# Optimization experiments

Measured on AMD Instinct MI355X. Metric: run time of the kernel, lower is better.

Reference implementation:

```python
import jax, jax.numpy as jnp
import numpy as np

B, N, D, H = 1, 4096, 1024, 16
HD = D // H  # head_dim = 64


def setup_inputs() -> dict:
    key = jax.random.key(0)
    ks = jax.random.split(key, 5)
    s = 0.02
    return {
        "x": jax.random.normal(ks[0], (B, N, D), dtype=jnp.float32),
        "Wq": jax.random.normal(ks[1], (D, D), dtype=jnp.float32) * s,
        "Wk": jax.random.normal(ks[2], (D, D), dtype=jnp.float32) * s,
        "Wv": jax.random.normal(ks[3], (D, D), dtype=jnp.float32) * s,
        "Wo": jax.random.normal(ks[4], (D, D), dtype=jnp.float32) * s,
        "bo": jnp.zeros((D,), dtype=jnp.float32),
    }


def reference(x, Wq, Wk, Wv, Wo, bo):
    b, n, d = x.shape
    # QKV projections -> [b, h, n, hd]
    def proj(W):
        return jnp.einsum("bnd,de->bne", x, W).reshape(b, n, H, HD).transpose(0, 2, 1, 3)
    q, k, v = proj(Wq), proj(Wk), proj(Wv)
    # Scores [b, h, n, n] with causal mask (matches masked_fill with triu(diag=1))
    scores = jnp.einsum("bhqd,bhkd->bhqk", q, k)
    causal = jnp.tril(jnp.ones((n, n), dtype=bool))
    scores = jnp.where(causal, scores, -jnp.inf)
    attn = jax.nn.softmax(scores / jnp.sqrt(jnp.float32(HD)), axis=-1)
    # dropout p=0.0 -> identity
    ctx = jnp.einsum("bhqk,bhkd->bhqd", attn, v)
    ctx = ctx.transpose(0, 2, 1, 3).reshape(b, n, d)
    return jnp.einsum("bnd,de->bne", ctx, Wo) + bo
```

## Files before the change

kernel.cpp:

```cpp
#include <hip/hip_runtime.h>


#define N_TOK 4096
#define DMODEL 1024
#define NH 16
#define HDIM 64

typedef __bf16 bf16x8 __attribute__((ext_vector_type(8)));
typedef short short4v __attribute__((ext_vector_type(4)));
typedef unsigned int uint2v __attribute__((ext_vector_type(2)));
typedef float f32x4 __attribute__((ext_vector_type(4)));

__device__ __forceinline__ unsigned short f2bf(float f) {
  unsigned u = __builtin_bit_cast(unsigned, f);
  u += 0x7FFFu + ((u >> 16) & 1u);
  return (unsigned short)(u >> 16);
}

__device__ __forceinline__ float bf2f(unsigned short u) {
  unsigned x = (unsigned)u << 16;
  return __builtin_bit_cast(float, x);
}

__device__ __forceinline__ unsigned pack2bf(float f0, float f1) {
  unsigned a = __builtin_bit_cast(unsigned, f0);
  unsigned b = __builtin_bit_cast(unsigned, f1);
  a += 0x7FFFu + ((a >> 16) & 1u);
  b += 0x7FFFu + ((b >> 16) & 1u);
  return (a >> 16) | (b & 0xFFFF0000u);
}

__device__ __forceinline__ f32x4 mfma16x16x16(short4v a, short4v b, f32x4 c) {
#if defined(__HIP_DEVICE_COMPILE__)
#if __has_builtin(__builtin_amdgcn_mfma_f32_16x16x16bf16_1k)
  return __builtin_amdgcn_mfma_f32_16x16x16bf16_1k(a, b, c, 0, 0, 0);
#else
  asm volatile("v_mfma_f32_16x16x16_bf16 %0, %1, %2, %0\n\ts_nop 7\n\ts_nop 1"
               : "+v"(c) : "v"(a), "v"(b));
  return c;
#endif
#else
  return c;
#endif
}

__device__ __forceinline__ void gll16(const unsigned short* g, unsigned short* l) {
#if defined(__HIP_DEVICE_COMPILE__)
  __builtin_amdgcn_global_load_lds((const __attribute__((address_space(1))) void*)g,
                                   (__attribute__((address_space(3))) void*)l, 16, 0, 0);
#endif
}

__global__ __launch_bounds__(256) void cast_x_kernel(const float* __restrict__ x,
                                                     unsigned short* __restrict__ xb) {
  const int i = (blockIdx.x * 256 + threadIdx.x) * 4;
  float4 v = *(const float4*)(x + i);
  ushort4 o;
  o.x = f2bf(v.x); o.y = f2bf(v.y); o.z = f2bf(v.z); o.w = f2bf(v.w);
  *(ushort4*)(xb + i) = o;
}

__global__ __launch_bounds__(256) void transpose_w_kernel(
    const float* __restrict__ Wq, const float* __restrict__ Wk,
    const float* __restrict__ Wv, const float* __restrict__ Wo,
    unsigned short* __restrict__ Wqt, unsigned short* __restrict__ Wkt,
    unsigned short* __restrict__ Wvt, unsigned short* __restrict__ Wot) {
  __shared__ float t[32][33];
  const float* src;
  unsigned short* dst;
  switch (blockIdx.z) {
    case 0: src = Wq; dst = Wqt; break;
    case 1: src = Wk; dst = Wkt; break;
    case 2: src = Wv; dst = Wvt; break;
    default: src = Wo; dst = Wot; break;
  }
  const int tx = threadIdx.x, ty = threadIdx.y;
  const int x = blockIdx.x * 32 + tx;
  const int y0 = blockIdx.y * 32;
#pragma unroll
  for (int i = 0; i < 32; i += 8) t[ty + i][tx] = src[(y0 + ty + i) * DMODEL + x];
  __syncthreads();
  const int ox = blockIdx.y * 32 + tx;
  const int oy0 = blockIdx.x * 32;
#pragma unroll
  for (int i = 0; i < 32; i += 8) dst[(oy0 + ty + i) * DMODEL + ox] = f2bf(t[tx][ty + i]);
}

__global__ __launch_bounds__(256) void gemm_qkv_kernel(
    const unsigned short* __restrict__ xb,
    const unsigned short* __restrict__ Wqt, const unsigned short* __restrict__ Wkt,
    const unsigned short* __restrict__ Wvt,
    unsigned short* __restrict__ Qg, unsigned short* __restrict__ Kg,
    unsigned short* __restrict__ Vg) {
  __shared__ unsigned short As[128 * 32];
  __shared__ unsigned short Bs[128 * 32];
  const int z = blockIdx.z;
  const unsigned short* Bmat = (z == 0) ? Wqt : ((z == 1) ? Wkt : Wvt);
  const int tid = threadIdx.x, lane = tid & 63, wv = tid >> 6;
  const int quad = lane >> 4, l15 = lane & 15;
  const int wm = wv >> 1, wn = wv & 1;
  const int tm0 = blockIdx.y * 128, tn0 = blockIdx.x * 128;
  const int lrow = lane >> 2, lcol = (lane & 3) * 8;
  const f32x4 zero4 = {0.f, 0.f, 0.f, 0.f};
  f32x4 acc[4][4];
#pragma unroll
  for (int i = 0; i < 4; ++i)
#pragma unroll
    for (int j = 0; j < 4; ++j) acc[i][j] = zero4;

  for (int kb = 0; kb < DMODEL; kb += 32) {
#pragma unroll
    for (int r = 0; r < 2; ++r) {
      const int row0 = r * 64 + wv * 16;
      gll16(&xb[(tm0 + row0 + lrow) * DMODEL + kb + lcol], &As[row0 * 32]);
      gll16(&Bmat[(tn0 + row0 + lrow) * DMODEL + kb + lcol], &Bs[row0 * 32]);
    }
    __syncthreads();
    bf16x8 af[4], bfr[4];
#pragma unroll
    for (int i = 0; i < 4; ++i) {
      af[i]  = *(const bf16x8*)&As[(wm * 64 + i * 16 + l15) * 32 + quad * 8];
      bfr[i] = *(const bf16x8*)&Bs[(wn * 64 + i * 16 + l15) * 32 + quad * 8];
    }
#pragma unroll
    for (int mt = 0; mt < 4; ++mt)
#pragma unroll
      for (int nt = 0; nt < 4; ++nt)
        acc[mt][nt] = __builtin_amdgcn_mfma_f32_16x16x32_bf16(af[mt], bfr[nt], acc[mt][nt], 0, 0, 0);
    __syncthreads();
  }

  const float qs = 0.125f * 1.44269504088896f;
#pragma unroll
  for (int mt = 0; mt < 4; ++mt)
#pragma unroll
    for (int nt = 0; nt < 4; ++nt)
#pragma unroll
      for (int r = 0; r < 4; ++r) {
        const int row = tm0 + wm * 64 + mt * 16 + quad * 4 + r;
        const int col = tn0 + wn * 64 + nt * 16 + l15;
        const float v = acc[mt][nt][r];
        const int hh = col >> 6, hd = col & 63;
        if (z == 0)      Qg[(hh * N_TOK + row) * HDIM + hd] = f2bf(v * qs);
        else if (z == 1) Kg[(hh * N_TOK + row) * HDIM + hd] = f2bf(v);
        else             Vg[(hh * N_TOK + row) * HDIM + hd] = f2bf(v);
      }
}

__global__ __launch_bounds__(256) void v_transpose_kernel(
    const unsigned short* __restrict__ Vg, unsigned short* __restrict__ Vtg) {
  __shared__ unsigned short t[64][72];
  const int h = blockIdx.y;
  const int n0 = blockIdx.x * 64;
  const int tx = threadIdx.x & 63, ty = threadIdx.x >> 6;
  const unsigned short* src = Vg + (h * N_TOK + n0) * HDIM;
#pragma unroll
  for (int i = 0; i < 64; i += 4) t[i + ty][tx] = src[(i + ty) * HDIM + tx];
  __syncthreads();
  unsigned short* dst = Vtg + h * HDIM * N_TOK + n0;
#pragma unroll
  for (int i = 0; i < 64; i += 4) dst[(i + ty) * N_TOK + tx] = t[tx][i + ty];
}

#define TRW 68

__device__ static const unsigned char T_TAB[63] = {
    10, 11, 12, 13, 14, 15, 16, 17, 18, 19, 20, 21, 22, 23, 24, 25, 26, 27, 28, 29, 30,
    31, 21, 22, 23, 24, 25, 26, 27, 28, 29, 30, 31,
    9, 20, 31, 8, 19, 30, 7, 18, 29, 6, 17, 28, 5, 16, 27,
    4, 15, 26, 3, 14, 25, 2, 13, 24, 1, 12, 23, 0, 11, 22};
__device__ static const unsigned char G_TAB[63] = {
    0, 0, 0, 0, 0, 0, 0, 0, 0, 0, 0, 0, 0, 0, 0, 0, 0, 0, 0, 0, 0,
    0, 1, 1, 1, 1, 1, 1, 1, 1, 1, 1, 1,
    0, 1, 2, 0, 1, 2, 0, 1, 2, 0, 1, 2, 0, 1, 2,
    0, 1, 2, 0, 1, 2, 0, 1, 2, 0, 1, 2, 0, 1, 2};

__device__ __forceinline__ void stage_kv(
    const unsigned short* __restrict__ Kh, const unsigned short* __restrict__ Vh,
    int kv0, char* buf, int wv, int lane) {
  unsigned short* Ksb = (unsigned short*)buf;
  unsigned short* Vsb = (unsigned short*)(buf + 8192);
  const int r8 = lane >> 3, g = lane & 7;
  const int sw = ((g ^ r8) * 8);
#pragma unroll
  for (int i = 0; i < 2; ++i) {
    const int row = wv * 16 + i * 8;
    gll16(&Kh[(kv0 + row + r8) * HDIM + sw], &Ksb[row * 64]);
    gll16(&Vh[(row + r8) * N_TOK + kv0 + sw], &Vsb[row * 64]);
  }
}

template <bool MASKED>
__device__ __forceinline__ void attn_step(
    int kvs, int qw, int quad, int l15,
    const unsigned short* __restrict__ Ks, const unsigned short* __restrict__ Vs,
    const bf16x8 (&qf)[2][2], f32x4 (&o)[2][4], float (&l_)[2]) {
  const f32x4 zero4 = {0.f, 0.f, 0.f, 0.f};
  const int s = l15 & 7;
  f32x4 c[2][4];
#pragma unroll
  for (int mt = 0; mt < 4; ++mt) {
    const unsigned short* kp = &Ks[(mt * 16 + l15) * 64];
    const int g0 = (quad ^ s) * 8;
    const bf16x8 kf0 = *(const bf16x8*)(kp + g0);
    const bf16x8 kf1 = *(const bf16x8*)(kp + (g0 ^ 32));
#pragma unroll
    for (int qt = 0; qt < 2; ++qt) {
      c[qt][mt] = __builtin_amdgcn_mfma_f32_16x16x32_bf16(kf0, qf[qt][0], zero4, 0, 0, 0);
      c[qt][mt] = __builtin_amdgcn_mfma_f32_16x16x32_bf16(kf1, qf[qt][1], c[qt][mt], 0, 0, 0);
    }
  }
  short4v pb[2][4];
#pragma unroll
  for (int qt = 0; qt < 2; ++qt) {
    const int q = qw + qt * 16 + l15;
    float ls = 0.f;
#pragma unroll
    for (int mt = 0; mt < 4; ++mt) {
      float p[4];
#pragma unroll
      for (int r = 0; r < 4; ++r) {
        float v = c[qt][mt][r];
        if (MASKED) v = ((kvs + mt * 16 + quad * 4 + r) <= q) ? v : -3e38f;
        p[r] = exp2f(v);
      }
      ls += (p[0] + p[1]) + (p[2] + p[3]);
      uint2v w;
      w.x = pack2bf(p[0], p[1]);
      w.y = pack2bf(p[2], p[3]);
      pb[qt][mt] = __builtin_bit_cast(short4v, w);
    }
    l_[qt] += ls;
  }
#pragma unroll
  for (int mt = 0; mt < 4; ++mt)
#pragma unroll
    for (int dt = 0; dt < 4; ++dt) {
      const int gv = (((2 * mt + (quad >> 1)) ^ s) * 8) + (quad & 1) * 4;
      const short4v vfx = *(const short4v*)&Vs[(dt * 16 + l15) * 64 + gv];
      o[0][dt] = mfma16x16x16(vfx, pb[0][mt], o[0][dt]);
      o[1][dt] = mfma16x16x16(vfx, pb[1][mt], o[1][dt]);
    }
}

__global__ __launch_bounds__(256, 3) void attn_kernel(
    const unsigned short* __restrict__ Qg, const unsigned short* __restrict__ Kg,
    const unsigned short* __restrict__ Vtg, unsigned short* __restrict__ ctx,
    unsigned short* __restrict__ part_o, float* __restrict__ part_l) {
  __shared__ __align__(16) char smem[34816];
  const int tid = threadIdx.x, lane = tid & 63, wv = tid >> 6;
  const int quad = lane >> 4, l15 = lane & 15;

  const int u = blockIdx.x >> 4;
  const int h = blockIdx.x & 15;
  const int t = T_TAB[u], g = G_TAB[u];
  const int c0 = g * 11;
  const int cend = (c0 + 10 < t) ? (c0 + 10) : t;
  const int mlen = 2 * (cend - c0 + 1);
  const bool multi = (t >= 11);
  const int qb = t * 128, qw = qb + wv * 32;

  const unsigned short* Qh = Qg + h * N_TOK * HDIM;
  const unsigned short* Kh = Kg + h * N_TOK * HDIM;
  const unsigned short* Vh = Vtg + h * HDIM * N_TOK;

  bf16x8 qf[2][2];
#pragma unroll
  for (int qt = 0; qt < 2; ++qt)
#pragma unroll
    for (int hh = 0; hh < 2; ++hh)
      qf[qt][hh] = *(const bf16x8*)&Qh[(qw + qt * 16 + l15) * HDIM + hh * 32 + quad * 8];

  const f32x4 zero4 = {0.f, 0.f, 0.f, 0.f};
  f32x4 o[2][4];
#pragma unroll
  for (int qt = 0; qt < 2; ++qt)
#pragma unroll
    for (int dt = 0; dt < 4; ++dt) o[qt][dt] = zero4;
  float l_[2] = {0.f, 0.f};

  const int kvbase = c0 << 7;
  stage_kv(Kh, Vh, kvbase, smem, wv, lane);
  int cur = 0;
#pragma unroll 1
  for (int mc = 0; mc < mlen; ++mc) {
    const int kv0 = kvbase + mc * 64;
    __syncthreads();
    if (mc + 1 < mlen)
      stage_kv(Kh, Vh, kv0 + 64, smem + (cur ^ 1) * 16384, wv, lane);
    const unsigned short* Ksb = (const unsigned short*)(smem + cur * 16384);
    const unsigned short* Vsb = (const unsigned short*)(smem + cur * 16384 + 8192);
    if (kv0 <= qw + 31) {
      if (kv0 + 63 <= qw)
        attn_step<false>(kv0, qw, quad, l15, Ksb, Vsb, qf, o, l_);
      else
        attn_step<true>(kv0, qw, quad, l15, Ksb, Vsb, qf, o, l_);
    }
    cur ^= 1;
  }
  __syncthreads();

  float* Tr = (float*)(smem + wv * (32 * TRW * 4));
  const int tq = lane >> 1, half = lane & 1;
  if (!multi) {
#pragma unroll
    for (int qt = 0; qt < 2; ++qt) {
      float l = l_[qt];
      l += __shfl_xor(l, 16, 64);
      l += __shfl_xor(l, 32, 64);
      const float inv = 1.0f / l;
#pragma unroll
      for (int dt = 0; dt < 4; ++dt) {
        f32x4 v = o[qt][dt] * inv;
        *(f32x4*)&Tr[(qt * 16 + l15) * TRW + dt * 16 + quad * 4] = v;
      }
    }
    unsigned short* dst = &ctx[(qb + wv * 32 + tq) * DMODEL + h * HDIM + half * 32];
    const float* src = &Tr[tq * TRW + half * 32];
#pragma unroll
    for (int j = 0; j < 4; ++j) {
      const float* s8 = src + j * 8;
      uint4 w;
      w.x = pack2bf(s8[0], s8[1]);
      w.y = pack2bf(s8[2], s8[3]);
      w.z = pack2bf(s8[4], s8[5]);
      w.w = pack2bf(s8[6], s8[7]);
      *(uint4*)(dst + j * 8) = w;
    }
  } else {
    const int slot = (h * 21 + (t - 11)) * 3 + g;
#pragma unroll
    for (int qt = 0; qt < 2; ++qt) {
      float l = l_[qt];
      l += __shfl_xor(l, 16, 64);
      l += __shfl_xor(l, 32, 64);
      if (quad == 0) part_l[slot * 128 + wv * 32 + qt * 16 + l15] = l;
#pragma unroll
      for (int dt = 0; dt < 4; ++dt)
        *(f32x4*)&Tr[(qt * 16 + l15) * TRW + dt * 16 + quad * 4] = o[qt][dt];
    }
    unsigned short* dst = part_o + (size_t)slot * 8192 + (wv * 32 + tq) * 64 + half * 32;
    const float* src = &Tr[tq * TRW + half * 32];
#pragma unroll
    for (int j = 0; j < 4; ++j) {
      const float* s8 = src + j * 8;
      uint4 w;
      w.x = pack2bf(s8[0], s8[1]);
      w.y = pack2bf(s8[2], s8[3]);
      w.z = pack2bf(s8[4], s8[5]);
      w.w = pack2bf(s8[6], s8[7]);
      *(uint4*)(dst + j * 8) = w;
    }
  }
}

__global__ __launch_bounds__(256) void merge_kernel(
    const unsigned short* __restrict__ part_o, const float* __restrict__ part_l,
    unsigned short* __restrict__ ctx) {
  const int b = blockIdx.x;
  const int h = b / 21, tt = b % 21;
  const int t = tt + 11;
  const int ng = t / 11 + 1;
  const int tid = threadIdx.x;
  const int q = tid >> 1, half = tid & 1;
  const int s0 = (h * 21 + tt) * 3;
  float l = 0.f;
  for (int g = 0; g < ng; ++g) l += part_l[(s0 + g) * 128 + q];
  const float inv = 1.0f / l;
  unsigned short* dst = &ctx[(t * 128 + q) * DMODEL + h * HDIM + half * 32];
#pragma unroll
  for (int j = 0; j < 4; ++j) {
    float acc[8] = {0.f, 0.f, 0.f, 0.f, 0.f, 0.f, 0.f, 0.f};
    for (int g = 0; g < ng; ++g) {
      const uint4 w = *(const uint4*)(part_o + (size_t)(s0 + g) * 8192 + q * 64 + half * 32 + j * 8);
      const unsigned short* us = (const unsigned short*)&w;
#pragma unroll
      for (int e = 0; e < 8; ++e) acc[e] += bf2f(us[e]);
    }
    uint4 w;
    w.x = pack2bf(acc[0] * inv, acc[1] * inv);
    w.y = pack2bf(acc[2] * inv, acc[3] * inv);
    w.z = pack2bf(acc[4] * inv, acc[5] * inv);
    w.w = pack2bf(acc[6] * inv, acc[7] * inv);
    *(uint4*)(dst + j * 8) = w;
  }
}

__global__ __launch_bounds__(256) void gemm_out_kernel(
    const unsigned short* __restrict__ ctxb, const unsigned short* __restrict__ Wot,
    const float* __restrict__ bo, float* __restrict__ out) {
  __shared__ unsigned short As[128 * 32];
  __shared__ unsigned short Bs[128 * 32];
  const int tid = threadIdx.x, lane = tid & 63, wv = tid >> 6;
  const int quad = lane >> 4, l15 = lane & 15;
  const int wm = wv >> 1, wn = wv & 1;
  const int tm0 = blockIdx.y * 128, tn0 = blockIdx.x * 128;
  const int lrow = lane >> 2, lcol = (lane & 3) * 8;
  const f32x4 zero4 = {0.f, 0.f, 0.f, 0.f};
  f32x4 acc[4][4];
#pragma unroll
  for (int i = 0; i < 4; ++i)
#pragma unroll
    for (int j = 0; j < 4; ++j) acc[i][j] = zero4;

  for (int kb = 0; kb < DMODEL; kb += 32) {
#pragma unroll
    for (int r = 0; r < 2; ++r) {
      const int row0 = r * 64 + wv * 16;
      gll16(&ctxb[(tm0 + row0 + lrow) * DMODEL + kb + lcol], &As[row0 * 32]);
      gll16(&Wot[(tn0 + row0 + lrow) * DMODEL + kb + lcol], &Bs[row0 * 32]);
    }
    __syncthreads();
    bf16x8 af[4], bfr[4];
#pragma unroll
    for (int i = 0; i < 4; ++i) {
      af[i]  = *(const bf16x8*)&As[(wm * 64 + i * 16 + l15) * 32 + quad * 8];
      bfr[i] = *(const bf16x8*)&Bs[(wn * 64 + i * 16 + l15) * 32 + quad * 8];
    }
#pragma unroll
    for (int mt = 0; mt < 4; ++mt)
#pragma unroll
      for (int nt = 0; nt < 4; ++nt)
        acc[mt][nt] = __builtin_amdgcn_mfma_f32_16x16x32_bf16(af[mt], bfr[nt], acc[mt][nt], 0, 0, 0);
    __syncthreads();
  }
#pragma unroll
  for (int mt = 0; mt < 4; ++mt)
#pragma unroll
    for (int nt = 0; nt < 4; ++nt)
#pragma unroll
      for (int r = 0; r < 4; ++r) {
        const int row = tm0 + wm * 64 + mt * 16 + quad * 4 + r;
        const int col = tn0 + wn * 64 + nt * 16 + l15;
        out[row * DMODEL + col] = acc[mt][nt][r] + bo[col];
      }
}

extern "C" void kernel_launch(void* const* d_in, const int* in_sizes, int n_in,
                              void* d_out, int out_size, void* d_ws, size_t ws_size,
                              hipStream_t stream) {
  const float* x  = (const float*)d_in[0];
  const float* Wq = (const float*)d_in[1];
  const float* Wk = (const float*)d_in[2];
  const float* Wv = (const float*)d_in[3];
  const float* Wo = (const float*)d_in[4];
  const float* bo = (const float*)d_in[5];
  float* out = (float*)d_out;

  char* ws = (char*)d_ws;
  unsigned short* xb  = (unsigned short*)(ws);
  unsigned short* Wqt = (unsigned short*)(ws + 8388608);
  unsigned short* Wkt = (unsigned short*)(ws + 8388608 + 2097152);
  unsigned short* Wvt = (unsigned short*)(ws + 8388608 + 2 * 2097152);
  unsigned short* Wot = (unsigned short*)(ws + 8388608 + 3 * 2097152);
  unsigned short* Qg  = (unsigned short*)(ws + 16777216);
  unsigned short* Kg  = (unsigned short*)(ws + 25165824);
  unsigned short* Vtg = (unsigned short*)(ws + 33554432);
  unsigned short* ctx = xb;
  unsigned short* part_o = (unsigned short*)(ws + 41943040);
  float* part_l = (float*)(ws + 58458112);
  unsigned short* Vg = part_o;

  cast_x_kernel<<<N_TOK * DMODEL / (256 * 4), 256, 0, stream>>>(x, xb);
  transpose_w_kernel<<<dim3(32, 32, 4), dim3(32, 8), 0, stream>>>(Wq, Wk, Wv, Wo, Wqt, Wkt, Wvt, Wot);
  gemm_qkv_kernel<<<dim3(DMODEL / 128, N_TOK / 128, 3), 256, 0, stream>>>(xb, Wqt, Wkt, Wvt, Qg, Kg, Vg);
  v_transpose_kernel<<<dim3(N_TOK / 64, NH), 256, 0, stream>>>(Vg, Vtg);
  attn_kernel<<<1008, 256, 0, stream>>>(Qg, Kg, Vtg, ctx, part_o, part_l);
  merge_kernel<<<336, 256, 0, stream>>>(part_o, part_l, ctx);
  gemm_out_kernel<<<dim3(DMODEL / 128, N_TOK / 128), 256, 0, stream>>>(ctx, Wot, bo, out);
}
```

Before: 242.0 us.

## Fuse prep kernels, write V transposed from QKV GEMM, use packed bf16 convert

Merges the x cast and weight transpose into one launch and drops the separate V transpose kernel: the QKV GEMM now transposes V tiles through shared memory and writes Vt directly with vector stores. The attention softmax also uses the hardware packed bf16 conversion when the builtin exists. This removes two kernel launches and a full round trip of V through global memory. The cost is extra shared memory (about 17KB) in the GEMM, which may lower its occupancy, plus added barriers in the V epilogue.

Result: faster. 235.4 us (-2.7%).

```diff
diff --git a/kernel.cpp b/kernel.cpp
--- a/kernel.cpp
+++ b/kernel.cpp
@@ -7,6 +7,7 @@
 #define HDIM 64
 
 typedef __bf16 bf16x8 __attribute__((ext_vector_type(8)));
+typedef __bf16 bf16x2v __attribute__((ext_vector_type(2)));
 typedef short short4v __attribute__((ext_vector_type(4)));
 typedef unsigned int uint2v __attribute__((ext_vector_type(2)));
 typedef float f32x4 __attribute__((ext_vector_type(4)));
@@ -28,6 +29,15 @@
   a += 0x7FFFu + ((a >> 16) & 1u);
   b += 0x7FFFu + ((b >> 16) & 1u);
   return (a >> 16) | (b & 0xFFFF0000u);
+}
+
+__device__ __forceinline__ unsigned packpk(float f0, float f1) {
+#if defined(__HIP_DEVICE_COMPILE__) && __has_builtin(__builtin_amdgcn_cvt_pk_bf16_f32)
+  bf16x2v r = __builtin_amdgcn_cvt_pk_bf16_f32(f0, f1);
+  return __builtin_bit_cast(unsigned, r);
+#else
+  return pack2bf(f0, f1);
+#endif
 }
 
 __device__ __forceinline__ f32x4 mfma16x16x16(short4v a, short4v b, f32x4 c) {
@@ -51,37 +61,41 @@
 #endif
 }
 
-__global__ __launch_bounds__(256) void cast_x_kernel(const float* __restrict__ x,
-                                                     unsigned short* __restrict__ xb) {
-  const int i = (blockIdx.x * 256 + threadIdx.x) * 4;
-  float4 v = *(const float4*)(x + i);
-  ushort4 o;
-  o.x = f2bf(v.x); o.y = f2bf(v.y); o.z = f2bf(v.z); o.w = f2bf(v.w);
-  *(ushort4*)(xb + i) = o;
-}
-
-__global__ __launch_bounds__(256) void transpose_w_kernel(
+__global__ __launch_bounds__(256) void prep_kernel(
+    const float* __restrict__ x, unsigned short* __restrict__ xb,
     const float* __restrict__ Wq, const float* __restrict__ Wk,
     const float* __restrict__ Wv, const float* __restrict__ Wo,
     unsigned short* __restrict__ Wqt, unsigned short* __restrict__ Wkt,
     unsigned short* __restrict__ Wvt, unsigned short* __restrict__ Wot) {
+  const int bx = blockIdx.x;
+  if (bx < 4096) {
+    const int i = (bx * 256 + threadIdx.x) * 4;
+    float4 v = *(const float4*)(x + i);
+    ushort4 o;
+    o.x = f2bf(v.x); o.y = f2bf(v.y); o.z = f2bf(v.z); o.w = f2bf(v.w);
+    *(ushort4*)(xb + i) = o;
+    return;
+  }
   __shared__ float t[32][33];
+  const int r = bx - 4096;
+  const int z = r >> 10, rem = r & 1023;
+  const int by = rem >> 5, bxx = rem & 31;
   const float* src;
   unsigned short* dst;
-  switch (blockIdx.z) {
+  switch (z) {
     case 0: src = Wq; dst = Wqt; break;
     case 1: src = Wk; dst = Wkt; break;
     case 2: src = Wv; dst = Wvt; break;
     default: src = Wo; dst = Wot; break;
   }
-  const int tx = threadIdx.x, ty = threadIdx.y;
-  const int x = blockIdx.x * 32 + tx;
-  const int y0 = blockIdx.y * 32;
-#pragma unroll
-  for (int i = 0; i < 32; i += 8) t[ty + i][tx] = src[(y0 + ty + i) * DMODEL + x];
+  const int tx = threadIdx.x & 31, ty = threadIdx.x >> 5;
+  const int xx = bxx * 32 + tx;
+  const int y0 = by * 32;
+#pragma unroll
+  for (int i = 0; i < 32; i += 8) t[ty + i][tx] = src[(y0 + ty + i) * DMODEL + xx];
   __syncthreads();
-  const int ox = blockIdx.y * 32 + tx;
-  const int oy0 = blockIdx.x * 32;
+  const int ox = by * 32 + tx;
+  const int oy0 = bxx * 32;
 #pragma unroll
   for (int i = 0; i < 32; i += 8) dst[(oy0 + ty + i) * DMODEL + ox] = f2bf(t[tx][ty + i]);
 }
@@ -91,9 +105,10 @@
     const unsigned short* __restrict__ Wqt, const unsigned short* __restrict__ Wkt,
     const unsigned short* __restrict__ Wvt,
     unsigned short* __restrict__ Qg, unsigned short* __restrict__ Kg,
-    unsigned short* __restrict__ Vg) {
+    unsigned short* __restrict__ Vtg) {
   __shared__ unsigned short As[128 * 32];
   __shared__ unsigned short Bs[128 * 32];
+  __shared__ unsigned short Tt[64 * 132];
   const int z = blockIdx.z;
   const unsigned short* Bmat = (z == 0) ? Wqt : ((z == 1) ? Wkt : Wvt);
   const int tid = threadIdx.x, lane = tid & 63, wv = tid >> 6;
@@ -131,35 +146,45 @@
   }
 
   const float qs = 0.125f * 1.44269504088896f;
-#pragma unroll
-  for (int mt = 0; mt < 4; ++mt)
-#pragma unroll
-    for (int nt = 0; nt < 4; ++nt)
-#pragma unroll
-      for (int r = 0; r < 4; ++r) {
-        const int row = tm0 + wm * 64 + mt * 16 + quad * 4 + r;
-        const int col = tn0 + wn * 64 + nt * 16 + l15;
-        const float v = acc[mt][nt][r];
-        const int hh = col >> 6, hd = col & 63;
-        if (z == 0)      Qg[(hh * N_TOK + row) * HDIM + hd] = f2bf(v * qs);
-        else if (z == 1) Kg[(hh * N_TOK + row) * HDIM + hd] = f2bf(v);
-        else             Vg[(hh * N_TOK + row) * HDIM + hd] = f2bf(v);
+  if (z < 2) {
+#pragma unroll
+    for (int mt = 0; mt < 4; ++mt)
+#pragma unroll
+      for (int nt = 0; nt < 4; ++nt)
+#pragma unroll
+        for (int r = 0; r < 4; ++r) {
+          const int row = tm0 + wm * 64 + mt * 16 + quad * 4 + r;
+          const int col = tn0 + wn * 64 + nt * 16 + l15;
+          const float v = acc[mt][nt][r];
+          const int hh = col >> 6, hd = col & 63;
+          if (z == 0) Qg[(hh * N_TOK + row) * HDIM + hd] = f2bf(v * qs);
+          else        Kg[(hh * N_TOK + row) * HDIM + hd] = f2bf(v);
+        }
+  } else {
+#pragma unroll 1
+    for (int p = 0; p < 2; ++p) {
+      if (wn == p) {
+#pragma unroll
+        for (int mt = 0; mt < 4; ++mt)
+#pragma unroll
+          for (int nt = 0; nt < 4; ++nt) {
+            const int c = nt * 16 + l15;
+#pragma unroll
+            for (int r = 0; r < 4; ++r)
+              Tt[c * 132 + wm * 64 + mt * 16 + quad * 4 + r] = f2bf(acc[mt][nt][r]);
+          }
       }
-}
-
-__global__ __launch_bounds__(256) void v_transpose_kernel(
-    const unsigned short* __restrict__ Vg, unsigned short* __restrict__ Vtg) {
-  __shared__ unsigned short t[64][72];
-  const int h = blockIdx.y;
-  const int n0 = blockIdx.x * 64;
-  const int tx = threadIdx.x & 63, ty = threadIdx.x >> 6;
-  const unsigned short* src = Vg + (h * N_TOK + n0) * HDIM;
-#pragma unroll
-  for (int i = 0; i < 64; i += 4) t[i + ty][tx] = src[(i + ty) * HDIM + tx];
-  __syncthreads();
-  unsigned short* dst = Vtg + h * HDIM * N_TOK + n0;
-#pragma unroll
-  for (int i = 0; i < 64; i += 4) dst[(i + ty) * N_TOK + tx] = t[tx][i + ty];
+      __syncthreads();
+      const int c = tid >> 2, seg = tid & 3;
+      const int hh = (tn0 + p * 64) >> 6;
+      unsigned short* dst = Vtg + hh * (HDIM * N_TOK) + c * N_TOK + tm0 + seg * 32;
+      const unsigned short* srcp = &Tt[c * 132 + seg * 32];
+#pragma unroll
+      for (int j = 0; j < 4; ++j)
+        *(uint4*)(dst + j * 8) = *(const uint4*)(srcp + j * 8);
+      __syncthreads();
+    }
+  }
 }
 
 #define TRW 68
@@ -226,8 +251,8 @@
       }
       ls += (p[0] + p[1]) + (p[2] + p[3]);
       uint2v w;
-      w.x = pack2bf(p[0], p[1]);
-      w.y = pack2bf(p[2], p[3]);
+      w.x = packpk(p[0], p[1]);
+      w.y = packpk(p[2], p[3]);
       pb[qt][mt] = __builtin_bit_cast(short4v, w);
     }
     l_[qt] += ls;
@@ -459,12 +484,9 @@
   unsigned short* ctx = xb;
   unsigned short* part_o = (unsigned short*)(ws + 41943040);
   float* part_l = (float*)(ws + 58458112);
-  unsigned short* Vg = part_o;
-
-  cast_x_kernel<<<N_TOK * DMODEL / (256 * 4), 256, 0, stream>>>(x, xb);
-  transpose_w_kernel<<<dim3(32, 32, 4), dim3(32, 8), 0, stream>>>(Wq, Wk, Wv, Wo, Wqt, Wkt, Wvt, Wot);
-  gemm_qkv_kernel<<<dim3(DMODEL / 128, N_TOK / 128, 3), 256, 0, stream>>>(xb, Wqt, Wkt, Wvt, Qg, Kg, Vg);
-  v_transpose_kernel<<<dim3(N_TOK / 64, NH), 256, 0, stream>>>(Vg, Vtg);
+
+  prep_kernel<<<8192, 256, 0, stream>>>(x, xb, Wq, Wk, Wv, Wo, Wqt, Wkt, Wvt, Wot);
+  gemm_qkv_kernel<<<dim3(DMODEL / 128, N_TOK / 128, 3), 256, 0, stream>>>(xb, Wqt, Wkt, Wvt, Qg, Kg, Vtg);
   attn_kernel<<<1008, 256, 0, stream>>>(Qg, Kg, Vtg, ctx, part_o, part_l);
   merge_kernel<<<336, 256, 0, stream>>>(part_o, part_l, ctx);
   gemm_out_kernel<<<dim3(DMODEL / 128, N_TOK / 128), 256, 0, stream>>>(ctx, Wot, bo, out);
```
